# Kernel optimization log

Hardware: AMD Instinct MI355X
Metric: run time of the kernel (lower is better)

## Reference

```python
import jax, jax.numpy as jnp
import numpy as np

N_NODES = 100000
N_EDGES = 1600000
IN_G = 128
IN_R = 64
HID = 128
N_GRAPHS = 512
BN_EPS = 1e-5


def _gcn_conv(x, W, b, src, dst, norm, n_nodes):
    # PyG GCNConv: h = X W; out[i] = sum_j norm_ij * h[j] over edges (incl. self-loops); + bias
    h = x @ W  # [N, C]
    msgs = h[src] * norm[:, None]  # [E', C]
    agg = jax.ops.segment_sum(msgs, dst, num_segments=n_nodes)
    return agg + b


def setup_inputs() -> dict:
    key = jax.random.key(0)
    ks = jax.random.split(key, 12)
    x = jax.random.normal(ks[0], (N_NODES, IN_G), dtype=jnp.float32)
    edge_index = jax.random.randint(ks[1], (2, N_EDGES), 0, N_NODES, dtype=jnp.int64)
    batch = jnp.sort(jax.random.randint(ks[2], (N_NODES,), 0, N_GRAPHS, dtype=jnp.int64))
    rst = jax.random.normal(ks[3], (N_GRAPHS, IN_R), dtype=jnp.float32)

    def lin(k, fan_in, fan_out):
        bound = 1.0 / np.sqrt(fan_in)
        k1, k2 = jax.random.split(k)
        W = jax.random.uniform(k1, (fan_in, fan_out), minval=-bound, maxval=bound, dtype=jnp.float32)
        b = jax.random.uniform(k2, (fan_out,), minval=-bound, maxval=bound, dtype=jnp.float32)
        return W, b

    W1, b1 = lin(ks[4], IN_G, HID)
    W2, b2 = lin(ks[5], HID, HID)
    Wg, bg = lin(ks[6], HID, HID // 2)
    Wr, br = lin(ks[7], IN_R, HID // 2)
    Wc, bc = lin(ks[8], HID, 2)
    gamma = jnp.ones((HID,), dtype=jnp.float32)
    beta = jnp.zeros((HID,), dtype=jnp.float32)
    return {"x": x, "edge_index": edge_index, "batch": batch, "rst": rst,
            "num_graphs": N_GRAPHS,
            "W1": W1, "b1": b1, "gamma": gamma, "beta": beta,
            "W2": W2, "b2": b2, "Wg": Wg, "bg": bg,
            "Wr": Wr, "br": br, "Wc": Wc, "bc": bc}


def reference(x, edge_index, batch, rst, num_graphs,
              W1, b1, gamma, beta, W2, b2, Wg, bg, Wr, br, Wc, bc):
    n = x.shape[0]
    # add self-loops (PyG GCNConv default)
    loop = jnp.arange(n, dtype=edge_index.dtype)
    src = jnp.concatenate([edge_index[0], loop])
    dst = jnp.concatenate([edge_index[1], loop])
    deg = jax.ops.segment_sum(jnp.ones_like(dst, dtype=x.dtype), dst, num_segments=n)
    dinv = jnp.where(deg > 0, jax.lax.rsqrt(deg), 0.0)
    norm = dinv[src] * dinv[dst]  # [E+N]

    h = _gcn_conv(x, W1, b1, src, dst, norm, n)
    # BatchNorm1d with batch statistics (training math; dropout omitted / eval)
    mu = jnp.mean(h, axis=0)
    var = jnp.var(h, axis=0)
    h = gamma * (h - mu) * jax.lax.rsqrt(var + BN_EPS) + beta
    h = jax.nn.relu(h)
    h = _gcn_conv(h, W2, b2, src, dst, norm, n)

    # global mean pool
    sums = jax.ops.segment_sum(h, batch, num_segments=num_graphs)
    counts = jax.ops.segment_sum(jnp.ones((n,), dtype=h.dtype), batch, num_segments=num_graphs)
    pooled = sums / jnp.maximum(counts, 1.0)[:, None]  # [G, HID]

    x_graph = jax.nn.relu(pooled @ Wg + bg)
    x_rst = jax.nn.relu(rst @ Wr + br)
    x_comb = jnp.concatenate([x_graph, x_rst], axis=1)
    return x_comb @ Wc + bc
```

## Files before the change

### kernel.cpp

```cpp
#include <hip/hip_runtime.h>


typedef __attribute__((ext_vector_type(8))) short bf16x8;
typedef __attribute__((ext_vector_type(4))) float f32x4;
typedef __attribute__((ext_vector_type(2))) float f32x2;
typedef __attribute__((ext_vector_type(2))) unsigned u32x2;
typedef __attribute__((ext_vector_type(4))) unsigned u32x4;

#define NBKT_MAX 256
#define BKT_SHIFT 9
#define TILE_E 4000
#define BSORT_CAP 4096
#define SRC_MASK 0x1FFFFu

__device__ __forceinline__ float bf_lo(unsigned u) {
  union { unsigned u; float f; } c; c.u = u << 16; return c.f;
}
__device__ __forceinline__ float bf_hi(unsigned u) {
  union { unsigned u; float f; } c; c.u = u & 0xffff0000u; return c.f;
}
__device__ __forceinline__ unsigned short f32_bf16(float f) {
  union { float f; unsigned u; } c; c.f = f;
  return (unsigned short)((c.u + 0x7fffu + ((c.u >> 16) & 1u)) >> 16);
}
__device__ __forceinline__ unsigned pack_bf16(float a, float b) {
  return (unsigned)f32_bf16(a) | ((unsigned)f32_bf16(b) << 16);
}
__device__ __forceinline__ unsigned pack_fp8x4(float c0, float c1, float c2, float c3) {
  int w = __builtin_amdgcn_cvt_pk_fp8_f32(c0, c1, 0, false);
  w = __builtin_amdgcn_cvt_pk_fp8_f32(c2, c3, w, true);
  return (unsigned)w;
}
__device__ __forceinline__ int aload(int* p) { return atomicAdd(p, 0); }

__global__ __launch_bounds__(256) void tile_hist_kernel(const int* __restrict__ dst,
                                                        int* __restrict__ tcnt,
                                                        int* __restrict__ counts,
                                                        float* __restrict__ stats,
                                                        const int* __restrict__ batch,
                                                        int* __restrict__ gstart,
                                                        int* __restrict__ syncp,
                                                        int e, int ntiles, int nbkt,
                                                        int n, int G) {
  __shared__ int hist[NBKT_MAX];
  int tile = blockIdx.x, tid = threadIdx.x;
  int idx = blockIdx.x * 256 + tid;
  if (idx < n) counts[idx] = 0;
  if (idx < 256) stats[idx] = 0.f;
  if (idx < 8) syncp[idx] = 0;
  if (idx <= G) {
    int g = idx;
    if (g == G) gstart[g] = n;
    else {
      int lo = 0, hi = n;
      while (lo < hi) {
        int mid = (lo + hi) >> 1;
        if (batch[mid] < g) lo = mid + 1; else hi = mid;
      }
      gstart[g] = lo;
    }
  }
  for (int b = tid; b < nbkt; b += 256) hist[b] = 0;
  __syncthreads();
  int t0 = tile * TILE_E;
  int tend = t0 + TILE_E; if (tend > e) tend = e;
  for (int i = t0 + tid; i < tend; i += 256)
    atomicAdd(&hist[__builtin_nontemporal_load(&dst[i]) >> BKT_SHIFT], 1);
  __syncthreads();
  for (int b = tid; b < nbkt; b += 256) tcnt[b * ntiles + tile] = hist[b];
}

__global__ __launch_bounds__(1024) void scan_ticket_kernel(const int* __restrict__ src,
                                                           int* __restrict__ dst,
                                                           int* __restrict__ bsum,
                                                           int* __restrict__ boff,
                                                           int* __restrict__ syncp,
                                                           float* __restrict__ dinv,
                                                           int n, int nb, int addone) {
  __shared__ int wsum[16];
  __shared__ int sflag, soff;
  int tid = threadIdx.x, lane = tid & 63, wid = tid >> 6;
  int bid = blockIdx.x;
  int idx = bid * 1024 + tid;
  int orig = (idx < n) ? (src[idx] + addone) : 0;
  if (dinv != nullptr && idx < n) dinv[idx] = rsqrtf((float)orig);
  int v = orig;
#pragma unroll
  for (int d = 1; d < 64; d <<= 1) {
    int t = __shfl_up(v, d, 64);
    if (lane >= d) v += t;
  }
  if (lane == 63) wsum[wid] = v;
  __syncthreads();
  if (wid == 0 && lane < 16) {
    int s = wsum[lane];
#pragma unroll
    for (int d = 1; d < 16; d <<= 1) {
      int t = __shfl_up(s, d, 64);
      if (lane >= d) s += t;
    }
    wsum[lane] = s;
  }
  __syncthreads();
  int wexcl = (wid == 0) ? 0 : wsum[wid - 1];
  int lexcl = wexcl + (v - orig);
  if (tid == 0) {
    atomicExch(&bsum[bid], wsum[15]);
    __threadfence();
    int t = atomicAdd(&syncp[0], 1);
    sflag = (t == nb - 1) ? 1 : 0;
  }
  __syncthreads();
  if (sflag) {
    if (tid < 64) {
      int base = tid * 4;
      int a0 = (base + 0 < nb) ? aload(&bsum[base + 0]) : 0;
      int a1 = (base + 1 < nb) ? aload(&bsum[base + 1]) : 0;
      int a2 = (base + 2 < nb) ? aload(&bsum[base + 2]) : 0;
      int a3 = (base + 3 < nb) ? aload(&bsum[base + 3]) : 0;
      int local = a0 + a1 + a2 + a3, s = local;
#pragma unroll
      for (int d = 1; d < 64; d <<= 1) {
        int t = __shfl_up(s, d, 64);
        if (tid >= d) s += t;
      }
      int excl = s - local;
      if (base + 0 < nb) atomicExch(&boff[base + 0], excl);
      if (base + 1 < nb) atomicExch(&boff[base + 1], excl + a0);
      if (base + 2 < nb) atomicExch(&boff[base + 2], excl + a0 + a1);
      if (base + 3 < nb) atomicExch(&boff[base + 3], excl + a0 + a1 + a2);
      __threadfence();
    }
    __syncthreads();
    if (tid == 0) atomicExch(&syncp[1], 1);
  }
  if (tid == 0) {
    while (aload(&syncp[1]) == 0) __builtin_amdgcn_s_sleep(8);
    soff = aload(&boff[bid]);
  }
  __syncthreads();
  if (idx < n) dst[idx] = soff + lexcl;
}

__global__ __launch_bounds__(256) void tile_scatter_kernel(const int* __restrict__ src,
                                                           const int* __restrict__ dst,
                                                           const int* __restrict__ tcnt,
                                                           const int* __restrict__ toff,
                                                           unsigned* __restrict__ pedge,
                                                           int e, int ntiles, int nbkt) {
  __shared__ int hb[NBKT_MAX], cnt[NBKT_MAX], gbase[NBKT_MAX];
  __shared__ unsigned led[TILE_E];
  __shared__ unsigned char bkt8[TILE_E];
  int tile = blockIdx.x, tid = threadIdx.x;
  for (int b = tid; b < nbkt; b += 256) {
    hb[b] = tcnt[b * ntiles + tile];
    gbase[b] = toff[b * ntiles + tile];
    cnt[b] = 0;
  }
  __syncthreads();
  if (tid < 64) {
    int b4 = tid * 4;
    int h0 = (b4 + 0 < nbkt) ? hb[b4 + 0] : 0;
    int h1 = (b4 + 1 < nbkt) ? hb[b4 + 1] : 0;
    int h2 = (b4 + 2 < nbkt) ? hb[b4 + 2] : 0;
    int h3 = (b4 + 3 < nbkt) ? hb[b4 + 3] : 0;
    int local = h0 + h1 + h2 + h3, v = local;
#pragma unroll
    for (int d = 1; d < 64; d <<= 1) {
      int t = __shfl_up(v, d, 64);
      if (tid >= d) v += t;
    }
    int excl = v - local;
    if (b4 + 0 < nbkt) hb[b4 + 0] = excl;
    if (b4 + 1 < nbkt) hb[b4 + 1] = excl + h0;
    if (b4 + 2 < nbkt) hb[b4 + 2] = excl + h0 + h1;
    if (b4 + 3 < nbkt) hb[b4 + 3] = excl + h0 + h1 + h2;
  }
  __syncthreads();
  int t0 = tile * TILE_E;
  int tend = t0 + TILE_E; if (tend > e) tend = e;
  for (int i = t0 + tid; i < tend; i += 256) {
    int s = __builtin_nontemporal_load(&src[i]);
    int d = __builtin_nontemporal_load(&dst[i]);
    int bkt = d >> BKT_SHIFT;
    int slot = hb[bkt] + atomicAdd(&cnt[bkt], 1);
    led[slot] = (unsigned)s | ((unsigned)(d & 511) << 17);
    bkt8[slot] = (unsigned char)bkt;
  }
  __syncthreads();
  int tc = tend - t0;
  for (int j = tid; j < tc; j += 256) {
    int bkt = bkt8[j];
    pedge[gbase[bkt] + (j - hb[bkt])] = led[j];
  }
}

__global__ __launch_bounds__(256) void deg_count_kernel(const unsigned* __restrict__ pedge,
                                                        const int* __restrict__ toff,
                                                        int* __restrict__ counts,
                                                        int e, int ntiles, int nbkt, int n) {
  __shared__ int cnt[512];
  int b = blockIdx.x >> 2, qu = blockIdx.x & 3;
  int nb0 = b << BKT_SHIFT;
  int nn = n - nb0; if (nn > 512) nn = 512;
  for (int l = threadIdx.x; l < 512; l += 256) cnt[l] = 0;
  __syncthreads();
  int estart = toff[b * ntiles];
  int eend = (b + 1 < nbkt) ? toff[(b + 1) * ntiles] : e;
  int len = eend - estart;
  int qb = estart + (int)((long long)len * qu / 4);
  int qe = estart + (int)((long long)len * (qu + 1) / 4);
  for (int i = qb + threadIdx.x; i < qe; i += 256)
    atomicAdd(&cnt[pedge[i] >> 17], 1);
  __syncthreads();
  for (int l = threadIdx.x; l < nn; l += 256) {
    int c = cnt[l];
    if (c) atomicAdd(&counts[nb0 + l], c);
  }
}

__global__ __launch_bounds__(256) void bucket_sort_kernel(const unsigned* __restrict__ pedge,
                                                          const int* __restrict__ toff,
                                                          const int* __restrict__ cursor,
                                                          int* __restrict__ sorted_src,
                                                          int e, int etot,
                                                          int ntiles, int nbkt, int n) {
  __shared__ int lcur[128];
  __shared__ int lsrc[BSORT_CAP];
  int b = blockIdx.x >> 2, qu = blockIdx.x & 3;
  int nb0 = b << BKT_SHIFT;
  int q0 = nb0 + qu * 128;
  if (q0 >= n) return;
  int q1 = q0 + 128; if (q1 > n) q1 = n;
  int qn = q1 - q0;
  int estart = toff[b * ntiles];
  int eend = (b + 1 < nbkt) ? toff[(b + 1) * ntiles] : e;
  int qstart = cursor[q0];
  int qend = (q1 < n) ? cursor[q1] : etot;
  unsigned qlo = (unsigned)(qu * 128);
  for (int l = threadIdx.x; l < qn; l += 256) lcur[l] = cursor[q0 + l] - qstart;
  __syncthreads();
  for (int i = estart + threadIdx.x; i < eend; i += 256) {
    unsigned p = pedge[i];
    unsigned rel = (p >> 17) - qlo;
    if (rel < (unsigned)qn) {
      int pos = atomicAdd(&lcur[rel], 1);
      if (pos < BSORT_CAP) lsrc[pos] = (int)(p & SRC_MASK);
    }
  }
  __syncthreads();
  for (int l = threadIdx.x; l < qn; l += 256) {
    int pos = lcur[l];
    if (pos < BSORT_CAP) lsrc[pos] = q0 + l;
  }
  __syncthreads();
  int qc = qend - qstart; if (qc > BSORT_CAP) qc = BSORT_CAP;
  for (int j = threadIdx.x; j < qc; j += 256) sorted_src[qstart + j] = lsrc[j];
}

template <int MODE>
__global__ __launch_bounds__(256) void gemm_mfma_kernel(const void* __restrict__ Ap,
                                                        const float* __restrict__ W,
                                                        const float* __restrict__ dinv,
                                                        const float* __restrict__ stats,
                                                        const float* __restrict__ gamma,
                                                        const float* __restrict__ beta,
                                                        unsigned* __restrict__ Cb, int n) {
  __shared__ unsigned short WB[16384];
  __shared__ float scs[128], shs[128];
  int tid = threadIdx.x;
  if (MODE == 1 && tid < 128) {
    float invN = 1.f / (float)n;
    float mu = stats[tid] * invN;
    float var = stats[128 + tid] * invN - mu * mu;
    float rstd = rsqrtf(var + 1e-5f);
    float s = gamma[tid] * rstd;
    scs[tid] = s;
    shs[tid] = beta[tid] - mu * s;
  }
  for (int t = tid; t < 2048; t += 256) {
    int nl = t & 15, ct = (t >> 4) & 7, qq = (t >> 7) & 3, kt = t >> 9;
    int c = ct * 16 + nl;
    int k0 = kt * 32 + qq * 8;
    union { bf16x8 v; unsigned short s[8]; } u;
#pragma unroll
    for (int j = 0; j < 8; ++j) u.s[j] = f32_bf16(W[(k0 + j) * 128 + c]);
    *(bf16x8*)&WB[(size_t)t * 8] = u.v;
  }
  __syncthreads();
  int lane = tid & 63;
  int m = lane & 15, q = lane >> 4;
  float scr[4][8], shr[4][8];
  if (MODE == 1) {
#pragma unroll
    for (int kt = 0; kt < 4; ++kt)
#pragma unroll
      for (int j = 0; j < 8; ++j) {
        int c = kt * 32 + q * 8 + j;
        scr[kt][j] = scs[c];
        shr[kt][j] = shs[c];
      }
  }
  int wv = (int)((blockIdx.x * 256u + tid) >> 6);
  int nwv = (int)((gridDim.x * 256u) >> 6);
  int ntl = n >> 4;
  if (wv >= ntl) return;
  f32x4 cf0, cf1, cf2, cf3, cf4, cf5, cf6, cf7;
  u32x4 cu0, cu1, cu2, cu3;
  {
    int row = wv * 16 + m;
    if (MODE == 1) {
      const u32x4* Au = (const u32x4*)((const unsigned*)Ap + (size_t)row * 64 + q * 4);
      cu0 = Au[0]; cu1 = Au[4]; cu2 = Au[8]; cu3 = Au[12];
    } else {
      const float* Ar = (const float*)Ap + (size_t)row * 128 + q * 8;
      cf0 = *(const f32x4*)(Ar);       cf1 = *(const f32x4*)(Ar + 4);
      cf2 = *(const f32x4*)(Ar + 32);  cf3 = *(const f32x4*)(Ar + 36);
      cf4 = *(const f32x4*)(Ar + 64);  cf5 = *(const f32x4*)(Ar + 68);
      cf6 = *(const f32x4*)(Ar + 96);  cf7 = *(const f32x4*)(Ar + 100);
    }
  }
  for (int t = wv; t < ntl; t += nwv) {
    int tn = t + nwv;
    f32x4 nf0, nf1, nf2, nf3, nf4, nf5, nf6, nf7;
    u32x4 nu0, nu1, nu2, nu3;
    if (tn < ntl) {
      int row = tn * 16 + m;
      if (MODE == 1) {
        const u32x4* Au = (const u32x4*)((const unsigned*)Ap + (size_t)row * 64 + q * 4);
        nu0 = Au[0]; nu1 = Au[4]; nu2 = Au[8]; nu3 = Au[12];
      } else {
        const float* Ar = (const float*)Ap + (size_t)row * 128 + q * 8;
        nf0 = *(const f32x4*)(Ar);       nf1 = *(const f32x4*)(Ar + 4);
        nf2 = *(const f32x4*)(Ar + 32);  nf3 = *(const f32x4*)(Ar + 36);
        nf4 = *(const f32x4*)(Ar + 64);  nf5 = *(const f32x4*)(Ar + 68);
        nf6 = *(const f32x4*)(Ar + 96);  nf7 = *(const f32x4*)(Ar + 100);
      }
    }
    bf16x8 af[4];
    if (MODE == 1) {
      u32x4 ww[4] = {cu0, cu1, cu2, cu3};
#pragma unroll
      for (int kt = 0; kt < 4; ++kt) {
        u32x4 w = ww[kt];
        float y0 = fmaxf(fmaf(scr[kt][0], bf_lo(w.x), shr[kt][0]), 0.f);
        float y1 = fmaxf(fmaf(scr[kt][1], bf_hi(w.x), shr[kt][1]), 0.f);
        float y2 = fmaxf(fmaf(scr[kt][2], bf_lo(w.y), shr[kt][2]), 0.f);
        float y3 = fmaxf(fmaf(scr[kt][3], bf_hi(w.y), shr[kt][3]), 0.f);
        float y4 = fmaxf(fmaf(scr[kt][4], bf_lo(w.z), shr[kt][4]), 0.f);
        float y5 = fmaxf(fmaf(scr[kt][5], bf_hi(w.z), shr[kt][5]), 0.f);
        float y6 = fmaxf(fmaf(scr[kt][6], bf_lo(w.w), shr[kt][6]), 0.f);
        float y7 = fmaxf(fmaf(scr[kt][7], bf_hi(w.w), shr[kt][7]), 0.f);
        union { bf16x8 v; unsigned uu[4]; } uf;
        uf.uu[0] = pack_bf16(y0, y1);
        uf.uu[1] = pack_bf16(y2, y3);
        uf.uu[2] = pack_bf16(y4, y5);
        uf.uu[3] = pack_bf16(y6, y7);
        af[kt] = uf.v;
      }
    } else {
      f32x4 lo[4] = {cf0, cf2, cf4, cf6};
      f32x4 hi[4] = {cf1, cf3, cf5, cf7};
#pragma unroll
      for (int kt = 0; kt < 4; ++kt) {
        f32x4 a0 = lo[kt], a1 = hi[kt];
        union { bf16x8 v; unsigned short s[8]; } u;
        u.s[0] = f32_bf16(a0.x); u.s[1] = f32_bf16(a0.y);
        u.s[2] = f32_bf16(a0.z); u.s[3] = f32_bf16(a0.w);
        u.s[4] = f32_bf16(a1.x); u.s[5] = f32_bf16(a1.y);
        u.s[6] = f32_bf16(a1.z); u.s[7] = f32_bf16(a1.w);
        af[kt] = u.v;
      }
    }
    f32x4 acc[8];
#pragma unroll
    for (int ct = 0; ct < 8; ++ct) acc[ct] = (f32x4){0.f, 0.f, 0.f, 0.f};
#pragma unroll
    for (int kt = 0; kt < 4; ++kt) {
#pragma unroll
      for (int ct = 0; ct < 8; ++ct) {
        bf16x8 b = *(const bf16x8*)&WB[(((kt * 4 + q) * 8 + ct) * 16 + m) * 8];
        acc[ct] = __builtin_amdgcn_mfma_f32_16x16x32_bf16(b, af[kt], acc[ct], 0, 0, 0);
      }
    }
    int row = t * 16 + m;
    float dv = dinv[row];
#pragma unroll
    for (int ct = 0; ct < 8; ++ct) {
      unsigned wout = pack_fp8x4(acc[ct][0] * dv, acc[ct][1] * dv,
                                 acc[ct][2] * dv, acc[ct][3] * dv);
      Cb[(size_t)row * 32 + ct * 4 + q] = wout;
    }
    if (MODE == 1) { cu0 = nu0; cu1 = nu1; cu2 = nu2; cu3 = nu3; }
    else { cf0 = nf0; cf1 = nf1; cf2 = nf2; cf3 = nf3;
           cf4 = nf4; cf5 = nf5; cf6 = nf6; cf7 = nf7; }
  }
}

__global__ __launch_bounds__(256) void gather_kernel(const unsigned* __restrict__ g,
    const int* __restrict__ srcs, const int* __restrict__ cursor,
    const int* __restrict__ counts, const float* __restrict__ dinv,
    unsigned* __restrict__ out, int n) {
  int lane = threadIdx.x & 63;
  int grp = lane >> 4;
  int sub = lane & 15;
  int gw = (int)((blockIdx.x * blockDim.x + threadIdx.x) >> 6);
  int nw = (int)((gridDim.x * blockDim.x) >> 6);
  for (int i0 = gw; i0 < n; i0 += nw) {
    int i = __builtin_amdgcn_readfirstlane(i0);
    int beg = cursor[i];
    int cnt2 = counts[i] + 1;
    float di = dinv[i];
    f32x2 A0 = {0.f, 0.f}, A1 = {0.f, 0.f}, A2 = {0.f, 0.f}, A3 = {0.f, 0.f};
#define ACC8(W0, W1)                                                       \
    { A0 += __builtin_amdgcn_cvt_pk_f32_fp8((int)(W0), false);             \
      A1 += __builtin_amdgcn_cvt_pk_f32_fp8((int)(W0), true);              \
      A2 += __builtin_amdgcn_cvt_pk_f32_fp8((int)(W1), false);             \
      A3 += __builtin_amdgcn_cvt_pk_f32_fp8((int)(W1), true); }
    int e = 0;
    for (; e + 16 <= cnt2; e += 16) {
      int sA = srcs[beg + e + grp];
      int sB = srcs[beg + e + grp + 4];
      int sC = srcs[beg + e + grp + 8];
      int sD = srcs[beg + e + grp + 12];
      u32x2 vA = *((const u32x2*)(g + ((size_t)sA << 5)) + sub);
      u32x2 vB = *((const u32x2*)(g + ((size_t)sB << 5)) + sub);
      u32x2 vC = *((const u32x2*)(g + ((size_t)sC << 5)) + sub);
      u32x2 vD = *((const u32x2*)(g + ((size_t)sD << 5)) + sub);
      ACC8(vA.x, vA.y) ACC8(vB.x, vB.y) ACC8(vC.x, vC.y) ACC8(vD.x, vD.y)
    }
    for (; e + 4 <= cnt2; e += 4) {
      int s = srcs[beg + e + grp];
      u32x2 v = *((const u32x2*)(g + ((size_t)s << 5)) + sub);
      ACC8(v.x, v.y)
    }
    if (e < cnt2) {
      int k = e + grp;
      int kk = (k < cnt2) ? k : cnt2 - 1;
      int s = srcs[beg + kk];
      float sel = (k < cnt2) ? 1.f : 0.f;
      u32x2 v = *((const u32x2*)(g + ((size_t)s << 5)) + sub);
      f32x2 p0 = __builtin_amdgcn_cvt_pk_f32_fp8((int)v.x, false);
      f32x2 p1 = __builtin_amdgcn_cvt_pk_f32_fp8((int)v.x, true);
      f32x2 p2 = __builtin_amdgcn_cvt_pk_f32_fp8((int)v.y, false);
      f32x2 p3 = __builtin_amdgcn_cvt_pk_f32_fp8((int)v.y, true);
      A0 += p0 * sel; A1 += p1 * sel; A2 += p2 * sel; A3 += p3 * sel;
    }
#undef ACC8
    float a0 = A0.x, a1 = A0.y, a2 = A1.x, a3 = A1.y;
    float a4 = A2.x, a5 = A2.y, a6 = A3.x, a7 = A3.y;
    a0 += __shfl_xor(a0, 16, 64); a0 += __shfl_xor(a0, 32, 64);
    a1 += __shfl_xor(a1, 16, 64); a1 += __shfl_xor(a1, 32, 64);
    a2 += __shfl_xor(a2, 16, 64); a2 += __shfl_xor(a2, 32, 64);
    a3 += __shfl_xor(a3, 16, 64); a3 += __shfl_xor(a3, 32, 64);
    a4 += __shfl_xor(a4, 16, 64); a4 += __shfl_xor(a4, 32, 64);
    a5 += __shfl_xor(a5, 16, 64); a5 += __shfl_xor(a5, 32, 64);
    a6 += __shfl_xor(a6, 16, 64); a6 += __shfl_xor(a6, 32, 64);
    a7 += __shfl_xor(a7, 16, 64); a7 += __shfl_xor(a7, 32, 64);
    if (grp == 0) {
      u32x4 o;
      o.x = pack_bf16(di * a0, di * a1);
      o.y = pack_bf16(di * a2, di * a3);
      o.z = pack_bf16(di * a4, di * a5);
      o.w = pack_bf16(di * a6, di * a7);
      *((u32x4*)(out + ((size_t)i << 6)) + sub) = o;
    }
  }
}

__global__ __launch_bounds__(256) void bn_stats_kernel(const unsigned* __restrict__ a,
                                                       float* __restrict__ stats, int n) {
  int c2 = threadIdx.x & 63;
  int ph = threadIdx.x >> 6;
  float s0 = 0.f, s1 = 0.f, q0 = 0.f, q1 = 0.f;
  for (int r = blockIdx.x * 4 + ph; r < n; r += gridDim.x * 4) {
    unsigned v = a[(size_t)r * 64 + c2];
    float x0 = bf_lo(v), x1 = bf_hi(v);
    s0 += x0; s1 += x1; q0 += x0 * x0; q1 += x1 * x1;
  }
  __shared__ float ls[4][64][4];
  ls[ph][c2][0] = s0; ls[ph][c2][1] = s1; ls[ph][c2][2] = q0; ls[ph][c2][3] = q1;
  __syncthreads();
  if (threadIdx.x < 64) {
    int c = threadIdx.x;
    float S0 = 0.f, S1 = 0.f, Q0 = 0.f, Q1 = 0.f;
#pragma unroll
    for (int p = 0; p < 4; ++p) {
      S0 += ls[p][c][0]; S1 += ls[p][c][1]; Q0 += ls[p][c][2]; Q1 += ls[p][c][3];
    }
    atomicAdd(&stats[2 * c], S0);
    atomicAdd(&stats[2 * c + 1], S1);
    atomicAdd(&stats[128 + 2 * c], Q0);
    atomicAdd(&stats[129 + 2 * c], Q1);
  }
}

__global__ __launch_bounds__(256) void poolhead_kernel(const unsigned* __restrict__ a,
    const int* __restrict__ gstart, const float* __restrict__ b2,
    const float* __restrict__ rst, const float* __restrict__ Wg,
    const float* __restrict__ bg, const float* __restrict__ Wr,
    const float* __restrict__ br, const float* __restrict__ Wc,
    const float* __restrict__ bc, float* __restrict__ out, int G) {
  int g = blockIdx.x;
  int t = threadIdx.x;
  int c2 = t & 63;
  int ph = t >> 6;
  int s = gstart[g], e = gstart[g + 1];
  float a0 = 0.f, a1 = 0.f;
  for (int r = s + ph; r < e; r += 4) {
    unsigned v = a[(size_t)r * 64 + c2];
    a0 += bf_lo(v); a1 += bf_hi(v);
  }
  __shared__ float ls[4][64][2];
  __shared__ float xp[128];
  __shared__ float xc[128];
  ls[ph][c2][0] = a0; ls[ph][c2][1] = a1;
  __syncthreads();
  if (t < 64) {
    int c = t;
    float S0 = 0.f, S1 = 0.f;
#pragma unroll
    for (int p = 0; p < 4; ++p) { S0 += ls[p][c][0]; S1 += ls[p][c][1]; }
    int cnt = e - s;
    float inv = (cnt > 0) ? 1.f / (float)cnt : 0.f;
    xp[2 * c]     = (cnt > 0) ? (S0 * inv + b2[2 * c]) : 0.f;
    xp[2 * c + 1] = (cnt > 0) ? (S1 * inv + b2[2 * c + 1]) : 0.f;
  }
  __syncthreads();
  if (t < 64) {
    float acc = bg[t];
    for (int k = 0; k < 128; ++k) acc = fmaf(xp[k], Wg[k * 64 + t], acc);
    xc[t] = fmaxf(acc, 0.f);
  } else if (t < 128) {
    int j = t - 64;
    float acc = br[j];
    const float* __restrict__ r = rst + (size_t)g * 64;
    for (int k = 0; k < 64; ++k) acc = fmaf(r[k], Wr[k * 64 + j], acc);
    xc[t] = fmaxf(acc, 0.f);
  }
  __syncthreads();
  if (t < 2) {
    float acc = bc[t];
    for (int j = 0; j < 128; ++j) acc = fmaf(xc[j], Wc[j * 2 + t], acc);
    out[(size_t)g * 2 + t] = acc;
  }
}

extern "C" void kernel_launch(void* const* d_in, const int* in_sizes, int n_in,
                              void* d_out, int out_size, void* d_ws, size_t ws_size,
                              hipStream_t stream) {
  (void)n_in; (void)ws_size;
  const float* x     = (const float*)d_in[0];
  const int*   ei    = (const int*)d_in[1];
  const int*   batch = (const int*)d_in[2];
  const float* rst   = (const float*)d_in[3];
  const float* W1    = (const float*)d_in[5];
  const float* gamma = (const float*)d_in[7];
  const float* beta  = (const float*)d_in[8];
  const float* W2    = (const float*)d_in[9];
  const float* b2    = (const float*)d_in[10];
  const float* Wg    = (const float*)d_in[11];
  const float* bg    = (const float*)d_in[12];
  const float* Wr    = (const float*)d_in[13];
  const float* br    = (const float*)d_in[14];
  const float* Wc    = (const float*)d_in[15];
  const float* bc    = (const float*)d_in[16];
  float* out = (float*)d_out;

  int N = in_sizes[0] / 128;
  int E = in_sizes[1] / 2;
  int G = out_size / 2;
  int ETOT = E + N;
  const int* esrc = ei;
  const int* edst = ei + E;

  int nbkt = (N + 511) >> BKT_SHIFT;
  int ntiles = (E + TILE_E - 1) / TILE_E;
  int tlen = nbkt * ntiles;

  char* ws = (char*)d_ws;
  size_t off = 0;
  auto alloc = [&](size_t bytes) -> void* {
    void* p = ws + off;
    off += (bytes + 255) & ~(size_t)255;
    return p;
  };
  unsigned* hb  = (unsigned*)alloc((size_t)N * 32 * 4);
  unsigned* agb = (unsigned*)alloc((size_t)N * 64 * 4);
  int* sorted   = (int*)alloc((size_t)ETOT * 4 + 256);
  unsigned* pedge = (unsigned*)alloc((size_t)E * 4);
  int* tcnt     = (int*)alloc((size_t)tlen * 4);
  int* toff     = (int*)alloc((size_t)tlen * 4);
  int* counts   = (int*)alloc((size_t)N * 4);
  int* cursor   = (int*)alloc((size_t)N * 4);
  float* dinv   = (float*)alloc((size_t)N * 4);
  float* stats  = (float*)alloc(256 * 4);
  int* gstart   = (int*)alloc((size_t)(G + 1) * 4);
  int* bsum     = (int*)alloc(256 * 4);
  int* boff     = (int*)alloc(256 * 4);
  int* syncp    = (int*)alloc(8 * 4);

  int nscan = (N + 1023) / 1024;
  int ntscan = (tlen + 1023) / 1024;
  int gblocks = (N / 16 + 7) / 8;

  tile_hist_kernel<<<ntiles, 256, 0, stream>>>(edst, tcnt, counts, stats, batch,
                                               gstart, syncp, E, ntiles, nbkt, N, G);
  scan_ticket_kernel<<<ntscan, 1024, 0, stream>>>(tcnt, toff, bsum, boff,
                                                  syncp, nullptr, tlen, ntscan, 0);
  tile_scatter_kernel<<<ntiles, 256, 0, stream>>>(esrc, edst, tcnt, toff, pedge,
                                                  E, ntiles, nbkt);
  deg_count_kernel<<<nbkt * 4, 256, 0, stream>>>(pedge, toff, counts, E, ntiles, nbkt, N);
  scan_ticket_kernel<<<nscan, 1024, 0, stream>>>(counts, cursor, bsum, boff,
                                                 syncp + 2, dinv, N, nscan, 1);
  bucket_sort_kernel<<<nbkt * 4, 256, 0, stream>>>(pedge, toff, cursor, sorted,
                                                   E, ETOT, ntiles, nbkt, N);

  gemm_mfma_kernel<0><<<gblocks, 256, 0, stream>>>(x, W1, dinv, stats, gamma, beta, hb, N);
  gather_kernel<<<4096, 256, 0, stream>>>(hb, sorted, cursor, counts, dinv, agb, N);

  bn_stats_kernel<<<512, 256, 0, stream>>>(agb, stats, N);

  gemm_mfma_kernel<1><<<gblocks, 256, 0, stream>>>(agb, W2, dinv, stats, gamma, beta, hb, N);
  gather_kernel<<<4096, 256, 0, stream>>>(hb, sorted, cursor, counts, dinv, agb, N);

  poolhead_kernel<<<G, 256, 0, stream>>>(agb, gstart, b2, rst, Wg, bg, Wr, br,
                                         Wc, bc, out, G);
}
```

Measured before the change: 367.8 us.

## Fuse BN statistics into first gather, widen bucket-sort blocks, resize GEMM grid

Measured after the change: 379.2 us. 3.1% more time.

```diff
diff --git a/kernel.cpp b/kernel.cpp
--- a/kernel.cpp
+++ b/kernel.cpp
@@ -10,7 +10,7 @@
 #define NBKT_MAX 256
 #define BKT_SHIFT 9
 #define TILE_E 4000
-#define BSORT_CAP 4096
+#define BSORT_CAP 6144
 #define SRC_MASK 0x1FFFFu
 
 __device__ __forceinline__ float bf_lo(unsigned u) {
@@ -225,19 +225,19 @@
                                                           int* __restrict__ sorted_src,
                                                           int e, int etot,
                                                           int ntiles, int nbkt, int n) {
-  __shared__ int lcur[128];
+  __shared__ int lcur[256];
   __shared__ int lsrc[BSORT_CAP];
-  int b = blockIdx.x >> 2, qu = blockIdx.x & 3;
+  int b = blockIdx.x >> 1, half = blockIdx.x & 1;
   int nb0 = b << BKT_SHIFT;
-  int q0 = nb0 + qu * 128;
+  int q0 = nb0 + half * 256;
   if (q0 >= n) return;
-  int q1 = q0 + 128; if (q1 > n) q1 = n;
+  int q1 = q0 + 256; if (q1 > n) q1 = n;
   int qn = q1 - q0;
   int estart = toff[b * ntiles];
   int eend = (b + 1 < nbkt) ? toff[(b + 1) * ntiles] : e;
   int qstart = cursor[q0];
   int qend = (q1 < n) ? cursor[q1] : etot;
-  unsigned qlo = (unsigned)(qu * 128);
+  unsigned qlo = (unsigned)(half * 256);
   for (int l = threadIdx.x; l < qn; l += 256) lcur[l] = cursor[q0 + l] - qstart;
   __syncthreads();
   for (int i = estart + threadIdx.x; i < eend; i += 256) {
@@ -397,14 +397,23 @@
   }
 }
 
+template <int STATS>
 __global__ __launch_bounds__(256) void gather_kernel(const unsigned* __restrict__ g,
     const int* __restrict__ srcs, const int* __restrict__ cursor,
     const int* __restrict__ counts, const float* __restrict__ dinv,
-    unsigned* __restrict__ out, int n) {
-  int lane = threadIdx.x & 63;
+    unsigned* __restrict__ out, float* __restrict__ stats, int n) {
+  __shared__ float bstat[256];
+  int tid = threadIdx.x;
+  int lane = tid & 63;
   int grp = lane >> 4;
   int sub = lane & 15;
-  int gw = (int)((blockIdx.x * blockDim.x + threadIdx.x) >> 6);
+  if (STATS) { bstat[tid] = 0.f; __syncthreads(); }
+  float st[8], sq[8];
+  if (STATS) {
+#pragma unroll
+    for (int j = 0; j < 8; ++j) { st[j] = 0.f; sq[j] = 0.f; }
+  }
+  int gw = (int)((blockIdx.x * blockDim.x + tid) >> 6);
   int nw = (int)((gridDim.x * blockDim.x) >> 6);
   for (int i0 = gw; i0 < n; i0 += nw) {
     int i = __builtin_amdgcn_readfirstlane(i0);
@@ -458,40 +467,32 @@
     a6 += __shfl_xor(a6, 16, 64); a6 += __shfl_xor(a6, 32, 64);
     a7 += __shfl_xor(a7, 16, 64); a7 += __shfl_xor(a7, 32, 64);
     if (grp == 0) {
+      float v0 = di * a0, v1 = di * a1, v2 = di * a2, v3 = di * a3;
+      float v4 = di * a4, v5 = di * a5, v6 = di * a6, v7 = di * a7;
+      if (STATS) {
+        st[0] += v0; sq[0] += v0 * v0; st[1] += v1; sq[1] += v1 * v1;
+        st[2] += v2; sq[2] += v2 * v2; st[3] += v3; sq[3] += v3 * v3;
+        st[4] += v4; sq[4] += v4 * v4; st[5] += v5; sq[5] += v5 * v5;
+        st[6] += v6; sq[6] += v6 * v6; st[7] += v7; sq[7] += v7 * v7;
+      }
       u32x4 o;
-      o.x = pack_bf16(di * a0, di * a1);
-      o.y = pack_bf16(di * a2, di * a3);
-      o.z = pack_bf16(di * a4, di * a5);
-      o.w = pack_bf16(di * a6, di * a7);
+      o.x = pack_bf16(v0, v1);
+      o.y = pack_bf16(v2, v3);
+      o.z = pack_bf16(v4, v5);
+      o.w = pack_bf16(v6, v7);
       *((u32x4*)(out + ((size_t)i << 6)) + sub) = o;
     }
   }
-}
-
-__global__ __launch_bounds__(256) void bn_stats_kernel(const unsigned* __restrict__ a,
-                                                       float* __restrict__ stats, int n) {
-  int c2 = threadIdx.x & 63;
-  int ph = threadIdx.x >> 6;
-  float s0 = 0.f, s1 = 0.f, q0 = 0.f, q1 = 0.f;
-  for (int r = blockIdx.x * 4 + ph; r < n; r += gridDim.x * 4) {
-    unsigned v = a[(size_t)r * 64 + c2];
-    float x0 = bf_lo(v), x1 = bf_hi(v);
-    s0 += x0; s1 += x1; q0 += x0 * x0; q1 += x1 * x1;
-  }
-  __shared__ float ls[4][64][4];
-  ls[ph][c2][0] = s0; ls[ph][c2][1] = s1; ls[ph][c2][2] = q0; ls[ph][c2][3] = q1;
-  __syncthreads();
-  if (threadIdx.x < 64) {
-    int c = threadIdx.x;
-    float S0 = 0.f, S1 = 0.f, Q0 = 0.f, Q1 = 0.f;
-#pragma unroll
-    for (int p = 0; p < 4; ++p) {
-      S0 += ls[p][c][0]; S1 += ls[p][c][1]; Q0 += ls[p][c][2]; Q1 += ls[p][c][3];
-    }
-    atomicAdd(&stats[2 * c], S0);
-    atomicAdd(&stats[2 * c + 1], S1);
-    atomicAdd(&stats[128 + 2 * c], Q0);
-    atomicAdd(&stats[129 + 2 * c], Q1);
+  if (STATS) {
+    if (grp == 0) {
+#pragma unroll
+      for (int j = 0; j < 8; ++j) {
+        atomicAdd(&bstat[8 * sub + j], st[j]);
+        atomicAdd(&bstat[128 + 8 * sub + j], sq[j]);
+      }
+    }
+    __syncthreads();
+    atomicAdd(&stats[tid], bstat[tid]);
   }
 }
 
@@ -602,7 +603,7 @@
 
   int nscan = (N + 1023) / 1024;
   int ntscan = (tlen + 1023) / 1024;
-  int gblocks = (N / 16 + 7) / 8;
+  int gblocks = (N / 16 + 15) / 16;
 
   tile_hist_kernel<<<ntiles, 256, 0, stream>>>(edst, tcnt, counts, stats, batch,
                                                gstart, syncp, E, ntiles, nbkt, N, G);
@@ -613,16 +614,16 @@
   deg_count_kernel<<<nbkt * 4, 256, 0, stream>>>(pedge, toff, counts, E, ntiles, nbkt, N);
   scan_ticket_kernel<<<nscan, 1024, 0, stream>>>(counts, cursor, bsum, boff,
                                                  syncp + 2, dinv, N, nscan, 1);
-  bucket_sort_kernel<<<nbkt * 4, 256, 0, stream>>>(pedge, toff, cursor, sorted,
+  bucket_sort_kernel<<<nbkt * 2, 256, 0, stream>>>(pedge, toff, cursor, sorted,
                                                    E, ETOT, ntiles, nbkt, N);
 
   gemm_mfma_kernel<0><<<gblocks, 256, 0, stream>>>(x, W1, dinv, stats, gamma, beta, hb, N);
-  gather_kernel<<<4096, 256, 0, stream>>>(hb, sorted, cursor, counts, dinv, agb, N);
-
-  bn_stats_kernel<<<512, 256, 0, stream>>>(agb, stats, N);
+  gather_kernel<1><<<2048, 256, 0, stream>>>(hb, sorted, cursor, counts, dinv,
+                                             agb, stats, N);
 
   gemm_mfma_kernel<1><<<gblocks, 256, 0, stream>>>(agb, W2, dinv, stats, gamma, beta, hb, N);
-  gather_kernel<<<4096, 256, 0, stream>>>(hb, sorted, cursor, counts, dinv, agb, N);
+  gather_kernel<0><<<4096, 256, 0, stream>>>(hb, sorted, cursor, counts, dinv,
+                                             agb, stats, N);
 
   poolhead_kernel<<<G, 256, 0, stream>>>(agb, gstart, b2, rst, Wg, bg, Wr, br,
                                          Wc, bc, out, G);
```

## Privatize BN stat atomics, widen bucket-sort chunks, and retune grid sizes

Applied to the files above, without the earlier changes.

Result: faster. 333.4 us (-9.3%).

```diff
diff --git a/kernel.cpp b/kernel.cpp
--- a/kernel.cpp
+++ b/kernel.cpp
@@ -10,8 +10,9 @@
 #define NBKT_MAX 256
 #define BKT_SHIFT 9
 #define TILE_E 4000
-#define BSORT_CAP 4096
+#define BSORT_CAP 6144
 #define SRC_MASK 0x1FFFFu
+#define SBKT 32
 
 __device__ __forceinline__ float bf_lo(unsigned u) {
   union { unsigned u; float f; } c; c.u = u << 16; return c.f;
@@ -36,7 +37,7 @@
 __global__ __launch_bounds__(256) void tile_hist_kernel(const int* __restrict__ dst,
                                                         int* __restrict__ tcnt,
                                                         int* __restrict__ counts,
-                                                        float* __restrict__ stats,
+                                                        float* __restrict__ stats_p,
                                                         const int* __restrict__ batch,
                                                         int* __restrict__ gstart,
                                                         int* __restrict__ syncp,
@@ -46,7 +47,7 @@
   int tile = blockIdx.x, tid = threadIdx.x;
   int idx = blockIdx.x * 256 + tid;
   if (idx < n) counts[idx] = 0;
-  if (idx < 256) stats[idx] = 0.f;
+  if (idx < SBKT * 256) stats_p[idx] = 0.f;
   if (idx < 8) syncp[idx] = 0;
   if (idx <= G) {
     int g = idx;
@@ -225,19 +226,19 @@
                                                           int* __restrict__ sorted_src,
                                                           int e, int etot,
                                                           int ntiles, int nbkt, int n) {
-  __shared__ int lcur[128];
+  __shared__ int lcur[256];
   __shared__ int lsrc[BSORT_CAP];
-  int b = blockIdx.x >> 2, qu = blockIdx.x & 3;
+  int b = blockIdx.x >> 1, half = blockIdx.x & 1;
   int nb0 = b << BKT_SHIFT;
-  int q0 = nb0 + qu * 128;
+  int q0 = nb0 + half * 256;
   if (q0 >= n) return;
-  int q1 = q0 + 128; if (q1 > n) q1 = n;
+  int q1 = q0 + 256; if (q1 > n) q1 = n;
   int qn = q1 - q0;
   int estart = toff[b * ntiles];
   int eend = (b + 1 < nbkt) ? toff[(b + 1) * ntiles] : e;
   int qstart = cursor[q0];
   int qend = (q1 < n) ? cursor[q1] : etot;
-  unsigned qlo = (unsigned)(qu * 128);
+  unsigned qlo = (unsigned)(half * 256);
   for (int l = threadIdx.x; l < qn; l += 256) lcur[l] = cursor[q0 + l] - qstart;
   __syncthreads();
   for (int i = estart + threadIdx.x; i < eend; i += 256) {
@@ -262,7 +263,7 @@
 __global__ __launch_bounds__(256) void gemm_mfma_kernel(const void* __restrict__ Ap,
                                                         const float* __restrict__ W,
                                                         const float* __restrict__ dinv,
-                                                        const float* __restrict__ stats,
+                                                        const float* __restrict__ stats_p,
                                                         const float* __restrict__ gamma,
                                                         const float* __restrict__ beta,
                                                         unsigned* __restrict__ Cb, int n) {
@@ -270,9 +271,15 @@
   __shared__ float scs[128], shs[128];
   int tid = threadIdx.x;
   if (MODE == 1 && tid < 128) {
+    float s0 = 0.f, s1 = 0.f;
+#pragma unroll 4
+    for (int k = 0; k < SBKT; ++k) {
+      s0 += stats_p[k * 256 + tid];
+      s1 += stats_p[k * 256 + 128 + tid];
+    }
     float invN = 1.f / (float)n;
-    float mu = stats[tid] * invN;
-    float var = stats[128 + tid] * invN - mu * mu;
+    float mu = s0 * invN;
+    float var = s1 * invN - mu * mu;
     float rstd = rsqrtf(var + 1e-5f);
     float s = gamma[tid] * rstd;
     scs[tid] = s;
@@ -469,7 +476,7 @@
 }
 
 __global__ __launch_bounds__(256) void bn_stats_kernel(const unsigned* __restrict__ a,
-                                                       float* __restrict__ stats, int n) {
+                                                       float* __restrict__ stats_p, int n) {
   int c2 = threadIdx.x & 63;
   int ph = threadIdx.x >> 6;
   float s0 = 0.f, s1 = 0.f, q0 = 0.f, q1 = 0.f;
@@ -488,10 +495,11 @@
     for (int p = 0; p < 4; ++p) {
       S0 += ls[p][c][0]; S1 += ls[p][c][1]; Q0 += ls[p][c][2]; Q1 += ls[p][c][3];
     }
-    atomicAdd(&stats[2 * c], S0);
-    atomicAdd(&stats[2 * c + 1], S1);
-    atomicAdd(&stats[128 + 2 * c], Q0);
-    atomicAdd(&stats[129 + 2 * c], Q1);
+    float* sp = stats_p + (blockIdx.x & (SBKT - 1)) * 256;
+    atomicAdd(&sp[2 * c], S0);
+    atomicAdd(&sp[2 * c + 1], S1);
+    atomicAdd(&sp[128 + 2 * c], Q0);
+    atomicAdd(&sp[129 + 2 * c], Q1);
   }
 }
 
@@ -594,7 +602,7 @@
   int* counts   = (int*)alloc((size_t)N * 4);
   int* cursor   = (int*)alloc((size_t)N * 4);
   float* dinv   = (float*)alloc((size_t)N * 4);
-  float* stats  = (float*)alloc(256 * 4);
+  float* stats_p = (float*)alloc((size_t)SBKT * 256 * 4);
   int* gstart   = (int*)alloc((size_t)(G + 1) * 4);
   int* bsum     = (int*)alloc(256 * 4);
   int* boff     = (int*)alloc(256 * 4);
@@ -602,9 +610,9 @@
 
   int nscan = (N + 1023) / 1024;
   int ntscan = (tlen + 1023) / 1024;
-  int gblocks = (N / 16 + 7) / 8;
-
-  tile_hist_kernel<<<ntiles, 256, 0, stream>>>(edst, tcnt, counts, stats, batch,
+  int gblocks = (N / 16 + 15) / 16;
+
+  tile_hist_kernel<<<ntiles, 256, 0, stream>>>(edst, tcnt, counts, stats_p, batch,
                                                gstart, syncp, E, ntiles, nbkt, N, G);
   scan_ticket_kernel<<<ntscan, 1024, 0, stream>>>(tcnt, toff, bsum, boff,
                                                   syncp, nullptr, tlen, ntscan, 0);
@@ -613,15 +621,15 @@
   deg_count_kernel<<<nbkt * 4, 256, 0, stream>>>(pedge, toff, counts, E, ntiles, nbkt, N);
   scan_ticket_kernel<<<nscan, 1024, 0, stream>>>(counts, cursor, bsum, boff,
                                                  syncp + 2, dinv, N, nscan, 1);
-  bucket_sort_kernel<<<nbkt * 4, 256, 0, stream>>>(pedge, toff, cursor, sorted,
+  bucket_sort_kernel<<<nbkt * 2, 256, 0, stream>>>(pedge, toff, cursor, sorted,
                                                    E, ETOT, ntiles, nbkt, N);
 
-  gemm_mfma_kernel<0><<<gblocks, 256, 0, stream>>>(x, W1, dinv, stats, gamma, beta, hb, N);
+  gemm_mfma_kernel<0><<<gblocks, 256, 0, stream>>>(x, W1, dinv, stats_p, gamma, beta, hb, N);
   gather_kernel<<<4096, 256, 0, stream>>>(hb, sorted, cursor, counts, dinv, agb, N);
 
-  bn_stats_kernel<<<512, 256, 0, stream>>>(agb, stats, N);
-
-  gemm_mfma_kernel<1><<<gblocks, 256, 0, stream>>>(agb, W2, dinv, stats, gamma, beta, hb, N);
+  bn_stats_kernel<<<1024, 256, 0, stream>>>(agb, stats_p, N);
+
+  gemm_mfma_kernel<1><<<gblocks, 256, 0, stream>>>(agb, W2, dinv, stats_p, gamma, beta, hb, N);
   gather_kernel<<<4096, 256, 0, stream>>>(hb, sorted, cursor, counts, dinv, agb, N);
 
   poolhead_kernel<<<G, 256, 0, stream>>>(agb, gstart, b2, rst, Wg, bg, Wr, br,
```
